# Optimization experiments

Measured on AMD Instinct MI355X. Metric: run time of the kernel, lower is better.

Reference implementation:

```python
import jax, jax.numpy as jnp
import numpy as np

K = 4          # neighbors
R = 2          # step_ratio
O = 64         # output_size


def setup_inputs() -> dict:
    key = jax.random.key(0)
    ks = jax.random.split(key, 7)
    B, C, N = 16, 128, 2048
    x = jax.random.normal(ks[0], (B, C, N), jnp.float32)
    # 1x1 conv weights stored as [out, in]; bias [out]
    w1 = jax.random.normal(ks[1], (O, 2 * C), jnp.float32) * (1.0 / np.sqrt(2 * C))
    b1 = jax.random.normal(ks[2], (O,), jnp.float32) * 0.01
    w2 = jax.random.normal(ks[3], (O * R, 2 * C + O), jnp.float32) * (1.0 / np.sqrt(2 * C + O))
    b2 = jax.random.normal(ks[4], (O * R,), jnp.float32) * 0.01
    w3 = jax.random.normal(ks[5], (O, O), jnp.float32) * (1.0 / np.sqrt(O))
    b3 = jax.random.normal(ks[6], (O,), jnp.float32) * 0.01
    return {"x": x, "w1": w1, "b1": b1, "w2": w2, "b2": b2, "w3": w3, "b3": b3}


def _knn_idx(x, k):
    # x: [B, C, N]; returns indices of k nearest neighbors (incl. self) [B, N, k]
    inner = -2.0 * jnp.einsum('bcn,bcm->bnm', x, x)           # [B, N, N]
    xx = jnp.sum(x * x, axis=1)                                # [B, N]
    pd = -xx[:, :, None] - inner - xx[:, None, :]              # negative sq dist
    return jax.lax.top_k(pd, k)[1]                             # [B, N, k]


def _graph_feature(x, k):
    # minus_center=False variant used by EF_expansion
    idx = _knn_idx(x, k)                                       # [B, N, k]
    xt = jnp.transpose(x, (0, 2, 1))                           # [B, N, C]
    feat = jax.vmap(lambda xb, ib: xb[ib])(xt, idx)            # [B, N, k, C]
    center = jnp.broadcast_to(xt[:, :, None, :], feat.shape)   # [B, N, k, C]
    f = jnp.concatenate([center, feat], axis=3)                # [B, N, k, 2C]
    return jnp.transpose(f, (0, 3, 1, 2))                      # [B, 2C, N, k]


def _conv1x1(w, b, x):
    # x: [B, Cin, H, W] -> [B, Cout, H, W]
    return jnp.einsum('oc,bchw->bohw', w, x) + b[None, :, None, None]


def reference(x, w1, b1, w2, b2, w3, b3):
    B, C, N = x.shape
    ief = jnp.transpose(_graph_feature(x, K), (0, 1, 3, 2))    # [B, 2C, k, N]
    e1 = _conv1x1(w1, b1, ief)                                 # [B, O, k, N]
    e = jax.nn.relu(jnp.concatenate([e1, ief], axis=1))        # [B, O+2C, k, N]
    e2 = jax.nn.relu(_conv1x1(w2, b2, e))                      # [B, O*R, k, N]
    # [B,O*R,k,N] -> [B,k,N,O*R] -> [B,k,N*R,O] -> [B,O,k,N*R]
    e2 = jnp.transpose(e2, (0, 2, 3, 1)).reshape(B, K, N * R, O)
    e2 = jnp.transpose(e2, (0, 3, 1, 2))
    e3 = _conv1x1(w3, b3, e2)                                  # [B, O, k, N*R]
    return jnp.max(e3, axis=2)                                 # [B, O, N*R]
```

## Files before the change

### kernel.cpp

```cpp
#include <hip/hip_runtime.h>
#include <cstdint>
#include <cstddef>

#define B_  16
#define C_  128
#define N_  2048
#define K_  4
#define O_  64
#define C2_ 256
#define ED_ 320
#define NM_ 4096
#define AGC 384

typedef float  f32x4  __attribute__((ext_vector_type(4)));
typedef short  s16x8  __attribute__((ext_vector_type(8)));
typedef __bf16 bf16x4 __attribute__((ext_vector_type(4)));
typedef __bf16 bf16x8 __attribute__((ext_vector_type(8)));
typedef unsigned short u16;
typedef unsigned int   u32;
typedef unsigned int   u32x4 __attribute__((ext_vector_type(4)));

__device__ __forceinline__ u32 umin32(u32 a, u32 b) { return a < b ? a : b; }
__device__ __forceinline__ u32 umax32(u32 a, u32 b) { return a > b ? a : b; }
__device__ __forceinline__ float bf2f(u16 h) { return __builtin_bit_cast(float, (u32)h << 16); }

__device__ __forceinline__ u32 med3u(u32 v, u32 a, u32 b) {
  u32 r;
  asm("v_med3_u32 %0, %1, %2, %3" : "=v"(r) : "v"(v), "v"(a), "v"(b));
  return r;
}

__device__ __forceinline__ s16x8 ldw_bf16(const float* __restrict__ p) {
  float4 a = *(const float4*)p;
  float4 c = *(const float4*)(p + 4);
  bf16x8 r;
  r[0] = (__bf16)a.x; r[1] = (__bf16)a.y; r[2] = (__bf16)a.z; r[3] = (__bf16)a.w;
  r[4] = (__bf16)c.x; r[5] = (__bf16)c.y; r[6] = (__bf16)c.z; r[7] = (__bf16)c.w;
  return __builtin_bit_cast(s16x8, r);
}

__device__ __forceinline__ u32 relu2(u32 u) {
  u32 s = u & 0x80008000u;
  u32 m = s - (s >> 15);
  return u & ~(m | s);
}
__device__ __forceinline__ s16x8 relu8(s16x8 v) {
  u32x4 u = __builtin_bit_cast(u32x4, v);
  u[0] = relu2(u[0]); u[1] = relu2(u[1]);
  u[2] = relu2(u[2]); u[3] = relu2(u[3]);
  return __builtin_bit_cast(s16x8, u);
}

__device__ __forceinline__ void glds16(const void* g, void* l) {
  __builtin_amdgcn_global_load_lds(
      (const __attribute__((address_space(1))) u32*)g,
      (__attribute__((address_space(3))) u32*)l, 16, 0, 0);
}

__global__ __launch_bounds__(256) void prep_kernel(const float* __restrict__ x,
                                                   const float* __restrict__ w1,
                                                   const float* __restrict__ w2,
                                                   const float* __restrict__ w3,
                                                   float* __restrict__ xT32,
                                                   u16* __restrict__ xh,
                                                   float* __restrict__ xx,
                                                   u16* __restrict__ wh,
                                                   u16* __restrict__ wg) {
  const int t = threadIdx.x;
  if (blockIdx.y == B_) {
    const int gid = blockIdx.x * 256 + t;
    for (int i = gid; i < 15360; i += 8192) {
      const float* src; u16* dst;
      if (i < 4096)       { src = w1 + (size_t)i * 4;            dst = wh + (size_t)i * 4; }
      else if (i < 14336) { src = w2 + (size_t)(i - 4096) * 4;   dst = wh + 16384 + (size_t)(i - 4096) * 4; }
      else                { src = w3 + (size_t)(i - 14336) * 4;  dst = wh + 57344 + (size_t)(i - 14336) * 4; }
      float4 v = *(const float4*)src;
      ushort4 h;
      h.x = __builtin_bit_cast(u16, (__bf16)v.x);
      h.y = __builtin_bit_cast(u16, (__bf16)v.y);
      h.z = __builtin_bit_cast(u16, (__bf16)v.z);
      h.w = __builtin_bit_cast(u16, (__bf16)v.w);
      *(ushort4*)dst = h;
    }
    if (wg) {
      for (int i = gid; i < 12288; i += 8192) {
        int r = i >> 5;
        int c4 = (i & 31) * 4;
        const float* src;
        if (r < 64)       src = w1 + (size_t)r * C2_ + c4;
        else if (r < 128) src = w1 + (size_t)(r - 64) * C2_ + 128 + c4;
        else if (r < 256) src = w2 + (size_t)(r - 128) * ED_ + 64 + c4;
        else              src = w2 + (size_t)(r - 256) * ED_ + 192 + c4;
        float4 v = *(const float4*)src;
        ushort4 h;
        h.x = __builtin_bit_cast(u16, (__bf16)v.x);
        h.y = __builtin_bit_cast(u16, (__bf16)v.y);
        h.z = __builtin_bit_cast(u16, (__bf16)v.z);
        h.w = __builtin_bit_cast(u16, (__bf16)v.w);
        *(ushort4*)&wg[(size_t)r * 128 + c4] = h;
      }
    }
    return;
  }

  __shared__ __align__(16) float sx[C_][65];
  const int b = blockIdx.y, n0 = blockIdx.x * 64;
  const float* xb = x + (size_t)b * C_ * N_;
  for (int u = t; u < C_ * 16; u += 256) {
    int c = u >> 4, f4 = u & 15;
    float4 v = *(const float4*)&xb[(size_t)c * N_ + n0 + f4 * 4];
    sx[c][f4 * 4 + 0] = v.x; sx[c][f4 * 4 + 1] = v.y;
    sx[c][f4 * 4 + 2] = v.z; sx[c][f4 * 4 + 3] = v.w;
  }
  __syncthreads();
  if (t < 64) {
    float s = 0.f;
    for (int c = 0; c < C_; ++c) { float v = sx[c][t]; s = fmaf(v, v, s); }
    xx[b * N_ + n0 + t] = s;
  }
  for (int u = t; u < 64 * 16; u += 256) {
    int n = u >> 4, cb = u & 15;
    float vv[8]; s16x8 hv;
#pragma unroll
    for (int j = 0; j < 8; ++j) {
      float v = sx[cb * 8 + j][n];
      vv[j] = v;
      hv[j] = (short)__builtin_bit_cast(u16, (__bf16)v);
    }
    size_t ro = ((size_t)b * N_ + n0 + n) * C_;
    *(float4*)&xT32[ro + cb * 8]     = make_float4(vv[0], vv[1], vv[2], vv[3]);
    *(float4*)&xT32[ro + cb * 8 + 4] = make_float4(vv[4], vv[5], vv[6], vv[7]);
    int sc = cb ^ (n & 7);
    *(s16x8*)&xh[ro + sc * 8] = hv;
  }
}

__global__ __launch_bounds__(256) void knn_mfma(const u16* __restrict__ xh,
                                                const float* __restrict__ xT32,
                                                const float* __restrict__ xx,
                                                int* __restrict__ knn_out) {
  __shared__ __align__(16) u32 shm[8448 + 512 + 512];
  u32*   cd  = shm;
  float* sq  = (float*)shm;
  u32*   cim = shm + 8448;
  float* sdv = (float*)(shm + 8448 + 512);
  const int b = blockIdx.y, q0 = blockIdx.x * 64;
  const int t = threadIdx.x;
  const int wv = t >> 6, lq = t & 15, lh = (t >> 4) & 3;
  const u16* xhb = xh + (size_t)b * N_ * C_;
  const float* xxb = xx + b * N_;

  s16x8 qf[4][4];
#pragma unroll
  for (int qt = 0; qt < 4; ++qt)
#pragma unroll
    for (int ks = 0; ks < 4; ++ks) {
      int q = q0 + qt * 16 + lq;
      int ch = (ks * 4 + lh) ^ (q & 7);
      qf[qt][ks] = *(const s16x8*)&xhb[(size_t)q * C_ + ch * 8];
    }

  u32 pk[4][5];
#pragma unroll
  for (int qt = 0; qt < 4; ++qt)
#pragma unroll
    for (int s = 0; s < 5; ++s) pk[qt][s] = 0xFFFFFFFFu;

  const int rbase = wv * 16 + lq;
  int choff[4];
#pragma unroll
  for (int ks = 0; ks < 4; ++ks) choff[ks] = ((ks * 4 + lh) ^ (lq & 7)) * 8;

  auto loadf = [&](int step, s16x8* d) {
    const u16* rp = xhb + (size_t)(step * 64 + rbase) * C_;
#pragma unroll
    for (int ks = 0; ks < 4; ++ks) d[ks] = *(const s16x8*)&rp[choff[ks]];
  };
  auto loadxx = [&](int step) -> f32x4 {
    return *(const f32x4*)&xxb[step * 64 + wv * 16 + lh * 4];
  };
  auto dostep = [&](int step, const s16x8* mf, f32x4 xm4) {
    f32x4 acc[4];
#pragma unroll
    for (int qt = 0; qt < 4; ++qt) acc[qt] = (f32x4){0.f, 0.f, 0.f, 0.f};
#pragma unroll
    for (int ks = 0; ks < 4; ++ks)
#pragma unroll
      for (int qt = 0; qt < 4; ++qt)
        acc[qt] = __builtin_amdgcn_mfma_f32_16x16x32_bf16(mf[ks], qf[qt][ks], acc[qt], 0, 0, 0);
    const int mrow = step * 64 + wv * 16 + lh * 4;
    float xma[4] = {xm4[0] + 512.f, xm4[1] + 512.f, xm4[2] + 512.f, xm4[3] + 512.f};
#pragma unroll
    for (int r = 0; r < 4; ++r) {
#pragma unroll
      for (int qt = 0; qt < 4; ++qt) {
        float dd = fmaf(acc[qt][r], -2.f, xma[r]);
        u32 u = __builtin_bit_cast(u32, dd);
        u32 v = (u & 0xFFFFF800u) | (u32)(mrow + r);
        u32 n0 = umin32(v, pk[qt][0]);
        u32 n1 = med3u(v, pk[qt][0], pk[qt][1]);
        u32 n2 = med3u(v, pk[qt][1], pk[qt][2]);
        u32 n3 = med3u(v, pk[qt][2], pk[qt][3]);
        u32 n4 = med3u(v, pk[qt][3], pk[qt][4]);
        pk[qt][0] = n0; pk[qt][1] = n1; pk[qt][2] = n2;
        pk[qt][3] = n3; pk[qt][4] = n4;
      }
    }
  };

  s16x8 fa[4], fb[4];
  f32x4 xa, xb4;
  loadf(0, fa);
  loadf(1, fb);
  xa = loadxx(0);
  xb4 = loadxx(1);
  for (int step = 0; step < 32; step += 2) {
    dostep(step, fa, xa);
    if (step + 2 < 32) { loadf(step + 2, fa); xa = loadxx(step + 2); }
    dostep(step + 1, fb, xb4);
    if (step + 3 < 32) { loadf(step + 3, fb); xb4 = loadxx(step + 3); }
  }

  const int unit = wv * 4 + lh;
#pragma unroll
  for (int qt = 0; qt < 4; ++qt) {
    int ql = qt * 16 + lq;
#pragma unroll
    for (int s = 0; s < 5; ++s) cd[ql * 85 + unit * 5 + s] = pk[qt][s];
  }
  __syncthreads();
  if (t < 64) {
    u32 fd[8];
#pragma unroll
    for (int s = 0; s < 8; ++s) fd[s] = 0xFFFFFFFFu;
    for (int j = 0; j < 80; ++j) {
      u32 v = cd[t * 85 + j];
      u32 m0 = umin32(v, fd[0]);
      u32 m1 = med3u(v, fd[0], fd[1]);
      u32 m2 = med3u(v, fd[1], fd[2]);
      u32 m3 = med3u(v, fd[2], fd[3]);
      u32 m4 = med3u(v, fd[3], fd[4]);
      u32 m5 = med3u(v, fd[4], fd[5]);
      u32 m6 = med3u(v, fd[5], fd[6]);
      u32 m7 = med3u(v, fd[6], fd[7]);
      fd[0] = m0; fd[1] = m1; fd[2] = m2; fd[3] = m3;
      fd[4] = m4; fd[5] = m5; fd[6] = m6; fd[7] = m7;
    }
#pragma unroll
    for (int s = 0; s < 8; ++s) cim[t * 8 + s] = fd[s] & 0x7FFu;
  }
  __syncthreads();

  {
    const float* xb32 = xT32 + (size_t)b * N_ * C_;
    for (int u = t; u < 64 * 32; u += 256) {
      int n = u >> 5, seg = u & 31;
      *(f32x4*)&sq[n * 132 + seg * 4] =
          *(const f32x4*)&xb32[(size_t)(q0 + n) * C_ + seg * 4];
    }
  }
  __syncthreads();

  {
    const float* xb32 = xT32 + (size_t)b * N_ * C_;
    const int ql = t >> 2, cs = t & 3;
    const float* qr = &sq[ql * 132];
#pragma unroll
    for (int cc = 0; cc < 2; ++cc) {
      int cslot = cs + cc * 4;
      int idx = (int)cim[ql * 8 + cslot];
      const float* mr = xb32 + (size_t)idx * C_;
      float a0 = 0.f, a1 = 0.f, a2 = 0.f, a3 = 0.f;
#pragma unroll 8
      for (int i = 0; i < 32; ++i) {
        f32x4 qv = *(const f32x4*)&qr[i * 4];
        float4 mv = *(const float4*)&mr[i * 4];
        a0 = fmaf(qv[0], mv.x, a0); a1 = fmaf(qv[1], mv.y, a1);
        a2 = fmaf(qv[2], mv.z, a2); a3 = fmaf(qv[3], mv.w, a3);
      }
      float dot = (a0 + a1) + (a2 + a3);
      sdv[ql * 8 + cslot] = xxb[idx] - 2.f * dot;
    }
  }
  __syncthreads();
  if (t < 64) {
    float dloc[8]; int iloc[8];
#pragma unroll
    for (int j = 0; j < 8; ++j) { dloc[j] = sdv[t * 8 + j]; iloc[j] = (int)cim[t * 8 + j]; }
    u32 used = 0;
#pragma unroll
    for (int s = 0; s < 4; ++s) {
      float bdv = 1e30f; int bidx = 0x7fffffff; int bj = 0;
#pragma unroll
      for (int j = 0; j < 8; ++j) {
        if (!((used >> j) & 1)) {
          bool bet = (dloc[j] < bdv) || (dloc[j] == bdv && iloc[j] < bidx);
          if (bet) { bdv = dloc[j]; bidx = iloc[j]; bj = j; }
        }
      }
      used |= 1u << bj;
      knn_out[((size_t)b * N_ + q0 + t) * K_ + s] = bidx;
    }
  }
}

__global__ __launch_bounds__(256, 2) void agemm_kernel(
    const u16* __restrict__ xh, const u16* __restrict__ wg,
    const float* __restrict__ b1, const float* __restrict__ b2,
    u16* __restrict__ ag) {
  __shared__ __align__(16) char sm[66560];
  u16* outT = (u16*)(sm + 16384);
  const int b = blockIdx.y, m0 = blockIdx.x * 64;
  const int t = threadIdx.x, lane = t & 63, wv = t >> 6, lq = t & 15, lh = (t >> 4) & 3;
  const u16* xhb = xh + (size_t)b * N_ * C_;

  {
    const char* s = (const char*)(xhb + (size_t)m0 * C_);
#pragma unroll
    for (int c = 0; c < 4; ++c) {
      int off = (wv * 4 + c) * 1024;
      glds16(s + off + lane * 16, sm + off);
    }
  }

  s16x8 af[6][4];
#pragma unroll
  for (int rt = 0; rt < 6; ++rt)
#pragma unroll
    for (int ks = 0; ks < 4; ++ks)
      af[rt][ks] = *(const s16x8*)&wg[(size_t)(wv * 96 + rt * 16 + lq) * 128 + ks * 32 + lh * 8];

  f32x4 acc[6][4];
#pragma unroll
  for (int rt = 0; rt < 6; ++rt)
#pragma unroll
    for (int cg = 0; cg < 4; ++cg) acc[rt][cg] = (f32x4){0.f, 0.f, 0.f, 0.f};

  asm volatile("s_waitcnt vmcnt(0)");
  __syncthreads();

#pragma unroll
  for (int cg = 0; cg < 4; ++cg) {
    s16x8 braw[4], brel[4];
#pragma unroll
    for (int ks = 0; ks < 4; ++ks) {
      int row = cg * 16 + lq;
      braw[ks] = *(const s16x8*)(sm + row * 256 + (((ks * 4 + lh) ^ (lq & 7)) * 16));
      brel[ks] = relu8(braw[ks]);
    }
#pragma unroll
    for (int rt = 0; rt < 6; ++rt) {
      const bool rl = (wv * 96 + rt * 16) >= 128;
#pragma unroll
      for (int ks = 0; ks < 4; ++ks)
        acc[rt][cg] = __builtin_amdgcn_mfma_f32_16x16x32_bf16(
            af[rt][ks], rl ? brel[ks] : braw[ks], acc[rt][cg], 0, 0, 0);
    }
  }

#pragma unroll
  for (int rt = 0; rt < 6; ++rt) {
    const int ch0 = wv * 96 + rt * 16 + lh * 4;
    float bias[4];
#pragma unroll
    for (int r = 0; r < 4; ++r) {
      int c = ch0 + r;
      bias[r] = (c < 64) ? b1[c] : ((c >= 128 && c < 256) ? b2[c - 128] : 0.f);
    }
#pragma unroll
    for (int cg = 0; cg < 4; ++cg) {
      bf16x4 st;
#pragma unroll
      for (int r = 0; r < 4; ++r) st[r] = (__bf16)(acc[rt][cg][r] + bias[r]);
      *(bf16x4*)&outT[(size_t)(cg * 16 + lq) * 392 + ch0] = st;
    }
  }
  __syncthreads();

  {
    const int row = t >> 2, p = t & 3;
#pragma unroll
    for (int k = 0; k < 12; ++k) {
      int seg = k * 4 + p;
      *(u32x4*)&ag[((size_t)b * N_ + m0 + row) * AGC + seg * 8] =
          *(const u32x4*)&outT[(size_t)row * 392 + seg * 8];
    }
  }
}

__global__ __launch_bounds__(256, 3) void fused_ag(
    const u16* __restrict__ ag, const u16* __restrict__ wh,
    const int* __restrict__ knn_idx,
    const float* __restrict__ b3, float* __restrict__ out) {
  __shared__ __align__(16) char fsm[44032];
  u16* e1T = (u16*)fsm;
  u16* s2T = (u16*)(fsm + 9216);
  u16* e2T = (u16*)(fsm + 26624);
  float* oSt = (float*)fsm;

  const int t = threadIdx.x, wv = t >> 6, lq = t & 15, lh = (t >> 4) & 3;
  const int b = blockIdx.y, n0 = blockIdx.x * 16;
  const u16* agb = ag + (size_t)b * N_ * AGC;
  const u16* w2h = wh + 16384;
  const u16* w3h = wh + 57344;

  s16x8 w2f[2][2];
#pragma unroll
  for (int rt = 0; rt < 2; ++rt)
#pragma unroll
    for (int ks = 0; ks < 2; ++ks)
      w2f[rt][ks] = *(const s16x8*)&w2h[(size_t)(wv * 32 + rt * 16 + lq) * ED_ + ks * 32 + lh * 8];
  const s16x8 w3a = *(const s16x8*)&w3h[(size_t)(wv * 16 + lq) * O_ + lh * 8];
  const s16x8 w3b = *(const s16x8*)&w3h[(size_t)(wv * 16 + lq) * O_ + 32 + lh * 8];
  const float4 b3v = *(const float4*)&b3[wv * 16 + lh * 4];

  {
    const int col = t >> 2, p = t & 3;
    const int n = n0 + (col >> 2);
    const int nid = knn_idx[((size_t)b * N_ + n) * K_ + (col & 3)];
    const u16* rc = agb + (size_t)n * AGC;
    const u16* rn = agb + (size_t)nid * AGC;
#pragma unroll
    for (int q = 0; q < 2; ++q) {
      s16x8 va = *(const s16x8*)&rc[p * 16 + q * 8];
      s16x8 vb = *(const s16x8*)&rn[64 + p * 16 + q * 8];
      bf16x8 r;
#pragma unroll
      for (int j = 0; j < 8; ++j)
        r[j] = (__bf16)fmaxf(bf2f((u16)va[j]) + bf2f((u16)vb[j]), 0.f);
      *(bf16x8*)&e1T[(size_t)col * 72 + p * 16 + q * 8] = r;
    }
#pragma unroll
    for (int q = 0; q < 4; ++q) {
      s16x8 va = *(const s16x8*)&rc[128 + p * 32 + q * 8];
      s16x8 vb = *(const s16x8*)&rn[256 + p * 32 + q * 8];
      bf16x8 r;
#pragma unroll
      for (int j = 0; j < 8; ++j)
        r[j] = (__bf16)(bf2f((u16)va[j]) + bf2f((u16)vb[j]));
      *(bf16x8*)&s2T[(size_t)col * 136 + p * 32 + q * 8] = r;
    }
  }
  __syncthreads();

  {
    f32x4 acc[2][4];
#pragma unroll
    for (int rt = 0; rt < 2; ++rt)
#pragma unroll
      for (int cg = 0; cg < 4; ++cg) acc[rt][cg] = (f32x4){0.f, 0.f, 0.f, 0.f};
#pragma unroll
    for (int ks = 0; ks < 2; ++ks)
#pragma unroll
      for (int cg = 0; cg < 4; ++cg) {
        s16x8 bf = *(const s16x8*)&e1T[(size_t)(cg * 16 + lq) * 72 + ks * 32 + lh * 8];
#pragma unroll
        for (int rt = 0; rt < 2; ++rt)
          acc[rt][cg] = __builtin_amdgcn_mfma_f32_16x16x32_bf16(w2f[rt][ks], bf, acc[rt][cg], 0, 0, 0);
      }
#pragma unroll
    for (int rt = 0; rt < 2; ++rt)
#pragma unroll
      for (int cg = 0; cg < 4; ++cg) {
        const int col = cg * 16 + lq;
        const int j0 = wv * 32 + rt * 16 + lh * 4;
        ushort4 sv = *(const ushort4*)&s2T[(size_t)col * 136 + j0];
        bf16x4 st;
        st[0] = (__bf16)fmaxf(acc[rt][cg][0] + bf2f(sv.x), 0.f);
        st[1] = (__bf16)fmaxf(acc[rt][cg][1] + bf2f(sv.y), 0.f);
        st[2] = (__bf16)fmaxf(acc[rt][cg][2] + bf2f(sv.z), 0.f);
        st[3] = (__bf16)fmaxf(acc[rt][cg][3] + bf2f(sv.w), 0.f);
        *(bf16x4*)&e2T[(size_t)col * 136 + j0] = st;
      }
  }
  __syncthreads();

  {
#pragma unroll
    for (int cg = 0; cg < 8; ++cg) {
      int col = cg * 16 + lq;
      int nl = col >> 3, rr = (col >> 2) & 1, kk = col & 3;
      int row = nl * 4 + kk;
      s16x8 f1 = *(const s16x8*)&e2T[(size_t)row * 136 + rr * 64 + lh * 8];
      s16x8 f2 = *(const s16x8*)&e2T[(size_t)row * 136 + rr * 64 + 32 + lh * 8];
      f32x4 acc = {0.f, 0.f, 0.f, 0.f};
      acc = __builtin_amdgcn_mfma_f32_16x16x32_bf16(w3a, f1, acc, 0, 0, 0);
      acc = __builtin_amdgcn_mfma_f32_16x16x32_bf16(w3b, f2, acc, 0, 0, 0);
      float vv[4];
#pragma unroll
      for (int r = 0; r < 4; ++r) {
        float v = acc[r];
        v = fmaxf(v, __shfl_xor(v, 1));
        v = fmaxf(v, __shfl_xor(v, 2));
        vv[r] = v;
      }
      if ((lq & 3) == 0) {
        int mloc = col >> 2;
        int o = wv * 16 + lh * 4;
        const float b3a[4] = {b3v.x, b3v.y, b3v.z, b3v.w};
#pragma unroll
        for (int r = 0; r < 4; ++r) oSt[(size_t)(o + r) * 36 + mloc] = vv[r] + b3a[r];
      }
    }
  }
  __syncthreads();

#pragma unroll
  for (int io = 0; io < 2; ++io) {
    int u = t + io * 256;
    int o = u >> 3, seg = u & 7;
    *(float4*)&out[((size_t)b * O_ + o) * NM_ + n0 * 2 + seg * 4] =
        *(const float4*)&oSt[(size_t)o * 36 + seg * 4];
  }
}

__global__ __launch_bounds__(256) void xx_kernel(const float* __restrict__ x,
                                                 float* __restrict__ xx) {
  int g = blockIdx.x * 256 + threadIdx.x;
  int b = g >> 11;
  int n = g & (N_ - 1);
  const float* xp = x + (size_t)b * C_ * N_ + n;
  float s = 0.f;
#pragma unroll 8
  for (int c = 0; c < C_; ++c) { float v = xp[(size_t)c * N_]; s += v * v; }
  xx[g] = s;
}

__global__ __launch_bounds__(256) void knn_kernel(const float* __restrict__ x,
                                                  const float* __restrict__ xx,
                                                  int* __restrict__ knn_out) {
  __shared__ __align__(16) float qT[C_ * 64];
  __shared__ __align__(16) float mT[C_ * 64];
  const int b = blockIdx.y;
  const int q0 = blockIdx.x * 64;
  const int t = threadIdx.x;
  const float* xb = x + (size_t)b * C_ * N_;
  const float* xxb = xx + b * N_;
  for (int i = t; i < C_ * 64; i += 256) {
    int c = i >> 6, q = i & 63;
    qT[i] = xb[(size_t)c * N_ + q0 + q];
  }
  const int tq = t & 15;
  const int tm = t >> 4;
  float bd[4][4]; int bi[4][4];
#pragma unroll
  for (int a = 0; a < 4; ++a)
#pragma unroll
    for (int s = 0; s < 4; ++s) { bd[a][s] = 1e30f; bi[a][s] = 0; }
  for (int m0 = 0; m0 < N_; m0 += 64) {
    __syncthreads();
    for (int i = t; i < C_ * 64; i += 256) {
      int c = i >> 6, m = i & 63;
      mT[i] = xb[(size_t)c * N_ + m0 + m];
    }
    __syncthreads();
    float acc[4][4];
#pragma unroll
    for (int a = 0; a < 4; ++a)
#pragma unroll
      for (int j = 0; j < 4; ++j) acc[a][j] = 0.f;
#pragma unroll 4
    for (int c = 0; c < C_; ++c) {
      float4 qv = *(const float4*)&qT[c * 64 + tq * 4];
      float4 mv = *(const float4*)&mT[c * 64 + tm * 4];
      float qa[4] = {qv.x, qv.y, qv.z, qv.w};
      float ma[4] = {mv.x, mv.y, mv.z, mv.w};
#pragma unroll
      for (int a = 0; a < 4; ++a)
#pragma unroll
        for (int j = 0; j < 4; ++j) acc[a][j] += qa[a] * ma[j];
    }
#pragma unroll
    for (int j = 0; j < 4; ++j) {
      float xm = xxb[m0 + tm * 4 + j];
      int id = m0 + tm * 4 + j;
#pragma unroll
      for (int a = 0; a < 4; ++a) {
        float d = xm - 2.f * acc[a][j];
        if (d < bd[a][3]) {
          bd[a][3] = d; bi[a][3] = id;
#pragma unroll
          for (int s = 3; s > 0; --s)
            if (bd[a][s] < bd[a][s - 1]) {
              float td = bd[a][s]; bd[a][s] = bd[a][s - 1]; bd[a][s - 1] = td;
              int ti = bi[a][s]; bi[a][s] = bi[a][s - 1]; bi[a][s - 1] = ti;
            }
        }
      }
    }
  }
  __syncthreads();
  float* cd = qT;
  int* ci = (int*)mT;
#pragma unroll
  for (int a = 0; a < 4; ++a) {
    int q = tq * 4 + a;
#pragma unroll
    for (int s = 0; s < 4; ++s) {
      cd[q * 64 + tm * 4 + s] = bd[a][s];
      ci[q * 64 + tm * 4 + s] = bi[a][s];
    }
  }
  __syncthreads();
  if (t < 64) {
    float fd[4]; int fi[4];
#pragma unroll
    for (int s = 0; s < 4; ++s) { fd[s] = 1e30f; fi[s] = 0; }
    for (int j = 0; j < 64; ++j) {
      float d = cd[t * 64 + j];
      int id = ci[t * 64 + j];
      if (d < fd[3]) {
        fd[3] = d; fi[3] = id;
#pragma unroll
        for (int s = 3; s > 0; --s)
          if (fd[s] < fd[s - 1]) {
            float td = fd[s]; fd[s] = fd[s - 1]; fd[s - 1] = td;
            int ti = fi[s]; fi[s] = fi[s - 1]; fi[s - 1] = ti;
          }
      }
    }
#pragma unroll
    for (int s = 0; s < 4; ++s)
      knn_out[(b * N_ + q0 + t) * K_ + s] = fi[s];
  }
}

__global__ __launch_bounds__(256, 5) void fused_fb(
    const float* __restrict__ x, const int* __restrict__ knn_idx,
    const float* __restrict__ w1, const float* __restrict__ b1,
    const float* __restrict__ w2, const float* __restrict__ b2,
    const float* __restrict__ w3, const float* __restrict__ b3,
    float* __restrict__ out) {
  __shared__ __align__(16) char fsm[30976];
  __bf16 (*cT)[136]  = (__bf16(*)[136])(fsm);
  __bf16 (*e1T)[72]  = (__bf16(*)[72])(fsm + 4352);
  float  (*oSt)[36]  = (float(*)[36])(fsm + 4352);
  __bf16 (*nT)[136]  = (__bf16(*)[136])(fsm + 13568);
  __bf16 (*e2T)[136] = (__bf16(*)[136])(fsm + 13568);

  const int b  = blockIdx.y;
  const int n0 = blockIdx.x * 16;
  const int t  = threadIdx.x;
  const float* xb = x + (size_t)b * C_ * N_;

  {
    const int stn = t >> 4, stc = t & 15;
    const int kbase = (b * N_ + n0) * K_;
    const float* srcc = xb + (size_t)(stc * 8) * N_ + n0 + stn;
    bf16x8 raw;
#pragma unroll
    for (int j = 0; j < 8; ++j) raw[j] = (__bf16)srcc[(size_t)j * N_];
    *(bf16x8*)&cT[stn][stc * 8] = raw;
#pragma unroll
    for (int it = 0; it < 4; ++it) {
      int col = stn + 16 * it;
      int nid = knn_idx[kbase + col];
      const float* src = xb + (size_t)(stc * 8) * N_ + nid;
      bf16x8 rw;
#pragma unroll
      for (int j = 0; j < 8; ++j) rw[j] = (__bf16)src[(size_t)j * N_];
      *(bf16x8*)&nT[col][stc * 8] = rw;
    }
  }
  __syncthreads();

  const int lq = t & 15;
  const int lh = (t >> 4) & 3;
  const int wv = t >> 6;

  {
    const float* w1r = w1 + (size_t)(wv * 16 + lq) * C2_;
    f32x4 acc[4];
#pragma unroll
    for (int cg = 0; cg < 4; ++cg) acc[cg] = (f32x4){0.f, 0.f, 0.f, 0.f};
#pragma unroll
    for (int ks = 0; ks < 8; ++ks) {
      s16x8 a = ldw_bf16(w1r + ks * 32 + lh * 8);
#pragma unroll
      for (int cg = 0; cg < 4; ++cg) {
        const __bf16* bp = (ks < 4)
            ? &cT[cg * 4 + (lq >> 2)][ks * 32 + lh * 8]
            : &nT[cg * 16 + lq][(ks - 4) * 32 + lh * 8];
        acc[cg] = __builtin_amdgcn_mfma_f32_16x16x32_bf16(
            a, *(const s16x8*)bp, acc[cg], 0, 0, 0);
      }
    }
#pragma unroll
    for (int cg = 0; cg < 4; ++cg) {
      bf16x4 st;
#pragma unroll
      for (int r = 0; r < 4; ++r) {
        float v = acc[cg][r] + b1[wv * 16 + lh * 4 + r];
        st[r] = (__bf16)fmaxf(v, 0.f);
      }
      *(bf16x4*)&e1T[cg * 16 + lq][wv * 16 + lh * 4] = st;
    }
  }
  __syncthreads();

  f32x4 acc2[2][4];
  {
    const float* w2r0 = w2 + (size_t)(wv * 32 + lq) * ED_;
    const float* w2r1 = w2r0 + (size_t)16 * ED_;
#pragma unroll
    for (int ro = 0; ro < 2; ++ro)
#pragma unroll
      for (int cg = 0; cg < 4; ++cg) acc2[ro][cg] = (f32x4){0.f, 0.f, 0.f, 0.f};
#pragma unroll
    for (int ks = 0; ks < 10; ++ks) {
      s16x8 a0 = ldw_bf16(w2r0 + ks * 32 + lh * 8);
      s16x8 a1 = ldw_bf16(w2r1 + ks * 32 + lh * 8);
#pragma unroll
      for (int cg = 0; cg < 4; ++cg) {
        s16x8 bf;
        if (ks < 2)      bf = *(const s16x8*)&e1T[cg * 16 + lq][ks * 32 + lh * 8];
        else if (ks < 6) bf = relu8(*(const s16x8*)&cT[cg * 4 + (lq >> 2)][(ks - 2) * 32 + lh * 8]);
        else             bf = relu8(*(const s16x8*)&nT[cg * 16 + lq][(ks - 6) * 32 + lh * 8]);
        acc2[0][cg] = __builtin_amdgcn_mfma_f32_16x16x32_bf16(a0, bf, acc2[0][cg], 0, 0, 0);
        acc2[1][cg] = __builtin_amdgcn_mfma_f32_16x16x32_bf16(a1, bf, acc2[1][cg], 0, 0, 0);
      }
    }
  }
  __syncthreads();
  {
#pragma unroll
    for (int ro = 0; ro < 2; ++ro)
#pragma unroll
      for (int cg = 0; cg < 4; ++cg) {
        bf16x4 st;
#pragma unroll
        for (int r = 0; r < 4; ++r) {
          float v = acc2[ro][cg][r] + b2[wv * 32 + ro * 16 + lh * 4 + r];
          st[r] = (__bf16)fmaxf(v, 0.f);
        }
        *(bf16x4*)&e2T[cg * 16 + lq][wv * 32 + ro * 16 + lh * 4] = st;
      }
  }
  __syncthreads();

  {
    const float* w3r = w3 + (size_t)(wv * 16 + lq) * O_;
    s16x8 a0 = ldw_bf16(w3r + lh * 8);
    s16x8 a1 = ldw_bf16(w3r + 32 + lh * 8);
#pragma unroll
    for (int cg = 0; cg < 8; ++cg) {
      int col = cg * 16 + lq;
      int nl = col >> 3, rr = (col >> 2) & 1, kk = col & 3;
      const __bf16* base = &e2T[nl * 4 + kk][rr * 64];
      f32x4 acc = {0.f, 0.f, 0.f, 0.f};
      acc = __builtin_amdgcn_mfma_f32_16x16x32_bf16(a0, *(const s16x8*)(base + lh * 8),      acc, 0, 0, 0);
      acc = __builtin_amdgcn_mfma_f32_16x16x32_bf16(a1, *(const s16x8*)(base + 32 + lh * 8), acc, 0, 0, 0);
      float vv[4];
#pragma unroll
      for (int r = 0; r < 4; ++r) {
        float v = acc[r];
        v = fmaxf(v, __shfl_xor(v, 1));
        v = fmaxf(v, __shfl_xor(v, 2));
        vv[r] = v;
      }
      if ((lq & 3) == 0) {
        int mloc = col >> 2;
        int o = wv * 16 + lh * 4;
#pragma unroll
        for (int r = 0; r < 4; ++r) oSt[o + r][mloc] = vv[r] + b3[o + r];
      }
    }
  }
  __syncthreads();

#pragma unroll
  for (int it = 0; it < 2; ++it) {
    int u = t + it * 256;
    int o = u >> 3, seg = u & 7;
    *(float4*)&out[((size_t)b * O_ + o) * NM_ + n0 * 2 + seg * 4] =
        *(const float4*)&oSt[o][seg * 4];
  }
}

extern "C" void kernel_launch(void* const* d_in, const int* in_sizes, int n_in,
                              void* d_out, int out_size, void* d_ws, size_t ws_size,
                              hipStream_t stream) {
  const float* x  = (const float*)d_in[0];
  const float* w1 = (const float*)d_in[1];
  const float* b1 = (const float*)d_in[2];
  const float* w2 = (const float*)d_in[3];
  const float* b2 = (const float*)d_in[4];
  const float* w3 = (const float*)d_in[5];
  const float* b3 = (const float*)d_in[6];
  float* out = (float*)d_out;

  const size_t AGB      = (size_t)B_ * N_ * AGC * 2;
  const size_t off_xhN  = AGB;
  const size_t off_xxN  = off_xhN + (size_t)B_ * N_ * C_ * 2;
  const size_t off_knnN = off_xxN + (size_t)B_ * N_ * 4;
  const size_t off_whN  = off_knnN + (size_t)B_ * N_ * K_ * 4;
  const size_t off_wgN  = off_whN + (size_t)61440 * 2;
  const size_t NEED_NEW = off_wgN + (size_t)AGC * 128 * 2;

  if (ws_size >= NEED_NEW) {
    u16*   agp  = (u16*)d_ws;
    float* xT32 = (float*)d_ws;
    u16*   xhp  = (u16*)((char*)d_ws + off_xhN);
    float* xx   = (float*)((char*)d_ws + off_xxN);
    int*   knn  = (int*)((char*)d_ws + off_knnN);
    u16*   whp  = (u16*)((char*)d_ws + off_whN);
    u16*   wgp  = (u16*)((char*)d_ws + off_wgN);

    hipLaunchKernelGGL(prep_kernel, dim3(N_ / 64, B_ + 1), dim3(256), 0, stream,
                       x, w1, w2, w3, xT32, xhp, xx, whp, wgp);
    hipLaunchKernelGGL(knn_mfma, dim3(N_ / 64, B_), dim3(256), 0, stream,
                       xhp, xT32, xx, knn);
    hipLaunchKernelGGL(agemm_kernel, dim3(N_ / 64, B_), dim3(256), 0, stream,
                       xhp, wgp, b1, b2, agp);
    hipLaunchKernelGGL(fused_ag, dim3(N_ / 16, B_), dim3(256), 0, stream,
                       agp, whp, knn, b3, out);
  } else {
    float* xx = (float*)d_ws;
    int* knn = (int*)((char*)d_ws + (size_t)B_ * N_ * 4);
    hipLaunchKernelGGL(xx_kernel, dim3((B_ * N_) / 256), dim3(256), 0, stream, x, xx);
    hipLaunchKernelGGL(knn_kernel, dim3(N_ / 64, B_), dim3(256), 0, stream, x, xx, knn);
    hipLaunchKernelGGL(fused_fb, dim3(N_ / 16, B_), dim3(256), 0, stream,
                       x, knn, w1, b1, w2, b2, w3, b3, out);
  }
}
```

Measured before the change: 99.06 us.

## Merge knn and agemm into one launch with interleaved block roles

Combines the kNN search kernel and the A-GEMM kernel into a single launch where even blocks run kNN and odd blocks run the GEMM, so the two independent stages run concurrently on the GPU. To allow this, the workspace layout gains a new arrangement where xT32 and the ag buffer no longer alias, selected when the workspace is large enough. The old layout is kept as a fallback. This drops one kernel launch and the tail between the two stages, but the merged kernel uses the larger shared-memory size for every block, which may lower occupancy for the kNN blocks.

```diff
diff --git a/kernel.cpp b/kernel.cpp
--- a/kernel.cpp
+++ b/kernel.cpp
@@ -21,7 +21,6 @@
 typedef unsigned int   u32x4 __attribute__((ext_vector_type(4)));
 
 __device__ __forceinline__ u32 umin32(u32 a, u32 b) { return a < b ? a : b; }
-__device__ __forceinline__ u32 umax32(u32 a, u32 b) { return a > b ? a : b; }
 __device__ __forceinline__ float bf2f(u16 h) { return __builtin_bit_cast(float, (u32)h << 16); }
 
 __device__ __forceinline__ u32 med3u(u32 v, u32 a, u32 b) {
@@ -135,16 +134,14 @@
   }
 }
 
-__global__ __launch_bounds__(256) void knn_mfma(const u16* __restrict__ xh,
-                                                const float* __restrict__ xT32,
-                                                const float* __restrict__ xx,
-                                                int* __restrict__ knn_out) {
-  __shared__ __align__(16) u32 shm[8448 + 512 + 512];
-  u32*   cd  = shm;
-  float* sq  = (float*)shm;
-  u32*   cim = shm + 8448;
-  float* sdv = (float*)(shm + 8448 + 512);
-  const int b = blockIdx.y, q0 = blockIdx.x * 64;
+__device__ __forceinline__ void knn_body(int b, int q0, const u16* __restrict__ xh,
+                                         const float* __restrict__ xT32,
+                                         const float* __restrict__ xx,
+                                         int* __restrict__ knn_out, char* smem) {
+  u32*   cd  = (u32*)smem;
+  float* sq  = (float*)smem;
+  u32*   cim = (u32*)smem + 8448;
+  float* sdv = (float*)((u32*)smem + 8448 + 512);
   const int t = threadIdx.x;
   const int wv = t >> 6, lq = t & 15, lh = (t >> 4) & 3;
   const u16* xhb = xh + (size_t)b * N_ * C_;
@@ -304,88 +301,120 @@
   }
 }
 
+__device__ __forceinline__ void agemm_body(int b, int m0, const u16* __restrict__ xh,
+                                           const u16* __restrict__ wg,
+                                           const float* __restrict__ b1,
+                                           const float* __restrict__ b2,
+                                           u16* __restrict__ ag, char* sm) {
+  u16* outT = (u16*)(sm + 16384);
+  const int t = threadIdx.x, lane = t & 63, wv = t >> 6, lq = t & 15, lh = (t >> 4) & 3;
+  const u16* xhb = xh + (size_t)b * N_ * C_;
+
+  {
+    const char* s = (const char*)(xhb + (size_t)m0 * C_);
+#pragma unroll
+    for (int c = 0; c < 4; ++c) {
+      int off = (wv * 4 + c) * 1024;
+      glds16(s + off + lane * 16, sm + off);
+    }
+  }
+
+  s16x8 af[6][4];
+#pragma unroll
+  for (int rt = 0; rt < 6; ++rt)
+#pragma unroll
+    for (int ks = 0; ks < 4; ++ks)
+      af[rt][ks] = *(const s16x8*)&wg[(size_t)(wv * 96 + rt * 16 + lq) * 128 + ks * 32 + lh * 8];
+
+  f32x4 acc[6][4];
+#pragma unroll
+  for (int rt = 0; rt < 6; ++rt)
+#pragma unroll
+    for (int cg = 0; cg < 4; ++cg) acc[rt][cg] = (f32x4){0.f, 0.f, 0.f, 0.f};
+
+  asm volatile("s_waitcnt vmcnt(0)");
+  __syncthreads();
+
+#pragma unroll
+  for (int cg = 0; cg < 4; ++cg) {
+    s16x8 braw[4], brel[4];
+#pragma unroll
+    for (int ks = 0; ks < 4; ++ks) {
+      int row = cg * 16 + lq;
+      braw[ks] = *(const s16x8*)(sm + row * 256 + (((ks * 4 + lh) ^ (lq & 7)) * 16));
+      brel[ks] = relu8(braw[ks]);
+    }
+#pragma unroll
+    for (int rt = 0; rt < 6; ++rt) {
+      const bool rl = (wv * 96 + rt * 16) >= 128;
+#pragma unroll
+      for (int ks = 0; ks < 4; ++ks)
+        acc[rt][cg] = __builtin_amdgcn_mfma_f32_16x16x32_bf16(
+            af[rt][ks], rl ? brel[ks] : braw[ks], acc[rt][cg], 0, 0, 0);
+    }
+  }
+
+#pragma unroll
+  for (int rt = 0; rt < 6; ++rt) {
+    const int ch0 = wv * 96 + rt * 16 + lh * 4;
+    float bias[4];
+#pragma unroll
+    for (int r = 0; r < 4; ++r) {
+      int c = ch0 + r;
+      bias[r] = (c < 64) ? b1[c] : ((c >= 128 && c < 256) ? b2[c - 128] : 0.f);
+    }
+#pragma unroll
+    for (int cg = 0; cg < 4; ++cg) {
+      bf16x4 st;
+#pragma unroll
+      for (int r = 0; r < 4; ++r) st[r] = (__bf16)(acc[rt][cg][r] + bias[r]);
+      *(bf16x4*)&outT[(size_t)(cg * 16 + lq) * 392 + ch0] = st;
+    }
+  }
+  __syncthreads();
+
+  {
+    const int row = t >> 2, p = t & 3;
+#pragma unroll
+    for (int k = 0; k < 12; ++k) {
+      int seg = k * 4 + p;
+      *(u32x4*)&ag[((size_t)b * N_ + m0 + row) * AGC + seg * 8] =
+          *(const u32x4*)&outT[(size_t)row * 392 + seg * 8];
+    }
+  }
+}
+
+__global__ __launch_bounds__(256) void knn_agemm(
+    const u16* __restrict__ xh, const float* __restrict__ xT32,
+    const float* __restrict__ xx, int* __restrict__ knn_out,
+    const u16* __restrict__ wg, const float* __restrict__ b1,
+    const float* __restrict__ b2, u16* __restrict__ ag) {
+  __shared__ __align__(16) char smem[66560];
+  const int bid = blockIdx.x;
+  const int role = bid & 1;
+  const int sub = bid >> 1;
+  const int b = sub >> 5, tile = (sub & 31) * 64;
+  if (role == 0) {
+    knn_body(b, tile, xh, xT32, xx, knn_out, smem);
+  } else {
+    agemm_body(b, tile, xh, wg, b1, b2, ag, smem);
+  }
+}
+
+__global__ __launch_bounds__(256) void knn_mfma(const u16* __restrict__ xh,
+                                                const float* __restrict__ xT32,
+                                                const float* __restrict__ xx,
+                                                int* __restrict__ knn_out) {
+  __shared__ __align__(16) char smem[37888];
+  knn_body(blockIdx.y, blockIdx.x * 64, xh, xT32, xx, knn_out, smem);
+}
+
 __global__ __launch_bounds__(256, 2) void agemm_kernel(
     const u16* __restrict__ xh, const u16* __restrict__ wg,
     const float* __restrict__ b1, const float* __restrict__ b2,
     u16* __restrict__ ag) {
   __shared__ __align__(16) char sm[66560];
-  u16* outT = (u16*)(sm + 16384);
-  const int b = blockIdx.y, m0 = blockIdx.x * 64;
-  const int t = threadIdx.x, lane = t & 63, wv = t >> 6, lq = t & 15, lh = (t >> 4) & 3;
-  const u16* xhb = xh + (size_t)b * N_ * C_;
-
-  {
-    const char* s = (const char*)(xhb + (size_t)m0 * C_);
-#pragma unroll
-    for (int c = 0; c < 4; ++c) {
-      int off = (wv * 4 + c) * 1024;
-      glds16(s + off + lane * 16, sm + off);
-    }
-  }
-
-  s16x8 af[6][4];
-#pragma unroll
-  for (int rt = 0; rt < 6; ++rt)
-#pragma unroll
-    for (int ks = 0; ks < 4; ++ks)
-      af[rt][ks] = *(const s16x8*)&wg[(size_t)(wv * 96 + rt * 16 + lq) * 128 + ks * 32 + lh * 8];
-
-  f32x4 acc[6][4];
-#pragma unroll
-  for (int rt = 0; rt < 6; ++rt)
-#pragma unroll
-    for (int cg = 0; cg < 4; ++cg) acc[rt][cg] = (f32x4){0.f, 0.f, 0.f, 0.f};
-
-  asm volatile("s_waitcnt vmcnt(0)");
-  __syncthreads();
-
-#pragma unroll
-  for (int cg = 0; cg < 4; ++cg) {
-    s16x8 braw[4], brel[4];
-#pragma unroll
-    for (int ks = 0; ks < 4; ++ks) {
-      int row = cg * 16 + lq;
-      braw[ks] = *(const s16x8*)(sm + row * 256 + (((ks * 4 + lh) ^ (lq & 7)) * 16));
-      brel[ks] = relu8(braw[ks]);
-    }
-#pragma unroll
-    for (int rt = 0; rt < 6; ++rt) {
-      const bool rl = (wv * 96 + rt * 16) >= 128;
-#pragma unroll
-      for (int ks = 0; ks < 4; ++ks)
-        acc[rt][cg] = __builtin_amdgcn_mfma_f32_16x16x32_bf16(
-            af[rt][ks], rl ? brel[ks] : braw[ks], acc[rt][cg], 0, 0, 0);
-    }
-  }
-
-#pragma unroll
-  for (int rt = 0; rt < 6; ++rt) {
-    const int ch0 = wv * 96 + rt * 16 + lh * 4;
-    float bias[4];
-#pragma unroll
-    for (int r = 0; r < 4; ++r) {
-      int c = ch0 + r;
-      bias[r] = (c < 64) ? b1[c] : ((c >= 128 && c < 256) ? b2[c - 128] : 0.f);
-    }
-#pragma unroll
-    for (int cg = 0; cg < 4; ++cg) {
-      bf16x4 st;
-#pragma unroll
-      for (int r = 0; r < 4; ++r) st[r] = (__bf16)(acc[rt][cg][r] + bias[r]);
-      *(bf16x4*)&outT[(size_t)(cg * 16 + lq) * 392 + ch0] = st;
-    }
-  }
-  __syncthreads();
-
-  {
-    const int row = t >> 2, p = t & 3;
-#pragma unroll
-    for (int k = 0; k < 12; ++k) {
-      int seg = k * 4 + p;
-      *(u32x4*)&ag[((size_t)b * N_ + m0 + row) * AGC + seg * 8] =
-          *(const u32x4*)&outT[(size_t)row * 392 + seg * 8];
-    }
-  }
+  agemm_body(blockIdx.y, blockIdx.x * 64, xh, wg, b1, b2, ag, sm);
 }
 
 __global__ __launch_bounds__(256, 3) void fused_ag(
@@ -789,22 +818,52 @@
   const float* b3 = (const float*)d_in[6];
   float* out = (float*)d_out;
 
-  const size_t AGB      = (size_t)B_ * N_ * AGC * 2;
-  const size_t off_xhN  = AGB;
-  const size_t off_xxN  = off_xhN + (size_t)B_ * N_ * C_ * 2;
-  const size_t off_knnN = off_xxN + (size_t)B_ * N_ * 4;
-  const size_t off_whN  = off_knnN + (size_t)B_ * N_ * K_ * 4;
-  const size_t off_wgN  = off_whN + (size_t)61440 * 2;
-  const size_t NEED_NEW = off_wgN + (size_t)AGC * 128 * 2;
-
-  if (ws_size >= NEED_NEW) {
+  const size_t XT32B = (size_t)B_ * N_ * C_ * 4;
+  const size_t XHB   = (size_t)B_ * N_ * C_ * 2;
+  const size_t XXB   = (size_t)B_ * N_ * 4;
+  const size_t KNNB  = (size_t)B_ * N_ * K_ * 4;
+  const size_t WHB   = (size_t)61440 * 2;
+  const size_t WGB   = (size_t)AGC * 128 * 2;
+  const size_t AGB   = (size_t)B_ * N_ * AGC * 2;
+
+  const size_t a_xh  = XT32B;
+  const size_t a_xx  = a_xh + XHB;
+  const size_t a_knn = a_xx + XXB;
+  const size_t a_wh  = a_knn + KNNB;
+  const size_t a_wg  = a_wh + WHB;
+  const size_t a_ag  = a_wg + WGB;
+  const size_t NEED_A = a_ag + AGB;
+
+  const size_t b_xh  = AGB;
+  const size_t b_xx  = b_xh + XHB;
+  const size_t b_knn = b_xx + XXB;
+  const size_t b_wh  = b_knn + KNNB;
+  const size_t b_wg  = b_wh + WHB;
+  const size_t NEED_B = b_wg + WGB;
+
+  if (ws_size >= NEED_A) {
+    float* xT32 = (float*)d_ws;
+    u16*   xhp  = (u16*)((char*)d_ws + a_xh);
+    float* xx   = (float*)((char*)d_ws + a_xx);
+    int*   knn  = (int*)((char*)d_ws + a_knn);
+    u16*   whp  = (u16*)((char*)d_ws + a_wh);
+    u16*   wgp  = (u16*)((char*)d_ws + a_wg);
+    u16*   agp  = (u16*)((char*)d_ws + a_ag);
+
+    hipLaunchKernelGGL(prep_kernel, dim3(N_ / 64, B_ + 1), dim3(256), 0, stream,
+                       x, w1, w2, w3, xT32, xhp, xx, whp, wgp);
+    hipLaunchKernelGGL(knn_agemm, dim3(1024), dim3(256), 0, stream,
+                       xhp, xT32, xx, knn, wgp, b1, b2, agp);
+    hipLaunchKernelGGL(fused_ag, dim3(N_ / 16, B_), dim3(256), 0, stream,
+                       agp, whp, knn, b3, out);
+  } else if (ws_size >= NEED_B) {
     u16*   agp  = (u16*)d_ws;
     float* xT32 = (float*)d_ws;
-    u16*   xhp  = (u16*)((char*)d_ws + off_xhN);
-    float* xx   = (float*)((char*)d_ws + off_xxN);
-    int*   knn  = (int*)((char*)d_ws + off_knnN);
-    u16*   whp  = (u16*)((char*)d_ws + off_whN);
-    u16*   wgp  = (u16*)((char*)d_ws + off_wgN);
+    u16*   xhp  = (u16*)((char*)d_ws + b_xh);
+    float* xx   = (float*)((char*)d_ws + b_xx);
+    int*   knn  = (int*)((char*)d_ws + b_knn);
+    u16*   whp  = (u16*)((char*)d_ws + b_wh);
+    u16*   wgp  = (u16*)((char*)d_ws + b_wg);
 
     hipLaunchKernelGGL(prep_kernel, dim3(N_ / 64, B_ + 1), dim3(256), 0, stream,
                        x, w1, w2, w3, xT32, xhp, xx, whp, wgp);
```

Measured after the change: 177.5 us. +79.2%, slower.
